# Performance work log

Measured on AMD Instinct MI355X. Metric: run time of the kernel, lower is better.

## Reference

```python
import jax, jax.numpy as jnp
import numpy as np

BATCH = 4096
VOCAB = 50257


def setup_inputs() -> dict:
    key = jax.random.key(0)
    k1, k2 = jax.random.split(key)
    pred = jax.random.normal(k1, (BATCH, VOCAB), dtype=jnp.float32)
    y = jax.random.randint(k2, (BATCH,), 0, VOCAB, dtype=jnp.int64)
    return {"pred": pred, "y": y}


def reference(pred, y):
    # Mean over batch of -log( exp(pred[i, y[i]]) / sum_j exp(pred[i, j]) )
    # == mean of -(log_softmax(pred)[i, y[i]]). Stable log-softmax is
    # mathematically identical to the original's unstabilized form.
    logp = jax.nn.log_softmax(pred, axis=-1)              # [B, V]
    picked = jnp.take_along_axis(logp, y[:, None], axis=-1)[:, 0]  # [B]
    return -jnp.mean(picked)
```

## Files before the change

### kernel.cpp

```cpp
#include <hip/hip_runtime.h>
#include <cstdint>

#define CE_BATCH 4096
#define CE_VOCAB 50257

__global__ __launch_bounds__(256, 4) void ce_kernel(const float* __restrict__ pred,
                                                    const int* __restrict__ y,
                                                    float* __restrict__ out) {
    const int b = blockIdx.x;
    const float* __restrict__ row = pred + (size_t)b * CE_VOCAB;
    const int tid = threadIdx.x;

    float m = -INFINITY;
    float s0 = 0.0f, s1 = 0.0f, s2 = 0.0f, s3 = 0.0f;
    float s4 = 0.0f, s5 = 0.0f, s6 = 0.0f, s7 = 0.0f;

    int lead = (int)(((16u - ((uintptr_t)row & 15u)) & 15u) >> 2);
    if (lead > CE_VOCAB) lead = CE_VOCAB;
    if (tid < lead) {
        m = row[tid];
        s0 = 1.0f;
    }

    const int nvec = (CE_VOCAB - lead) >> 2;
    const float4* __restrict__ vrow = (const float4*)(row + lead);

    int i = tid;
    for (; i + 7 * 256 < nvec; i += 8 * 256) {
        float4 v0 = vrow[i];
        float4 v1 = vrow[i + 1 * 256];
        float4 v2 = vrow[i + 2 * 256];
        float4 v3 = vrow[i + 3 * 256];
        float4 v4 = vrow[i + 4 * 256];
        float4 v5 = vrow[i + 5 * 256];
        float4 v6 = vrow[i + 6 * 256];
        float4 v7 = vrow[i + 7 * 256];

        float m0 = fmaxf(fmaxf(v0.x, v0.y), fmaxf(v0.z, v0.w));
        float m1 = fmaxf(fmaxf(v1.x, v1.y), fmaxf(v1.z, v1.w));
        float m2 = fmaxf(fmaxf(v2.x, v2.y), fmaxf(v2.z, v2.w));
        float m3 = fmaxf(fmaxf(v3.x, v3.y), fmaxf(v3.z, v3.w));
        float m4 = fmaxf(fmaxf(v4.x, v4.y), fmaxf(v4.z, v4.w));
        float m5 = fmaxf(fmaxf(v5.x, v5.y), fmaxf(v5.z, v5.w));
        float m6 = fmaxf(fmaxf(v6.x, v6.y), fmaxf(v6.z, v6.w));
        float m7 = fmaxf(fmaxf(v7.x, v7.y), fmaxf(v7.z, v7.w));
        float g = fmaxf(fmaxf(fmaxf(m0, m1), fmaxf(m2, m3)),
                        fmaxf(fmaxf(m4, m5), fmaxf(m6, m7)));

        if (g > m) {
            float r = __expf(m - g);
            s0 *= r; s1 *= r; s2 *= r; s3 *= r;
            s4 *= r; s5 *= r; s6 *= r; s7 *= r;
            m = g;
        }

        s0 += (__expf(v0.x - m) + __expf(v0.y - m)) + (__expf(v0.z - m) + __expf(v0.w - m));
        s1 += (__expf(v1.x - m) + __expf(v1.y - m)) + (__expf(v1.z - m) + __expf(v1.w - m));
        s2 += (__expf(v2.x - m) + __expf(v2.y - m)) + (__expf(v2.z - m) + __expf(v2.w - m));
        s3 += (__expf(v3.x - m) + __expf(v3.y - m)) + (__expf(v3.z - m) + __expf(v3.w - m));
        s4 += (__expf(v4.x - m) + __expf(v4.y - m)) + (__expf(v4.z - m) + __expf(v4.w - m));
        s5 += (__expf(v5.x - m) + __expf(v5.y - m)) + (__expf(v5.z - m) + __expf(v5.w - m));
        s6 += (__expf(v6.x - m) + __expf(v6.y - m)) + (__expf(v6.z - m) + __expf(v6.w - m));
        s7 += (__expf(v7.x - m) + __expf(v7.y - m)) + (__expf(v7.z - m) + __expf(v7.w - m));
    }

    for (; i < nvec; i += 256) {
        float4 v = vrow[i];
        float g = fmaxf(fmaxf(v.x, v.y), fmaxf(v.z, v.w));
        if (g > m) {
            float r = __expf(m - g);
            s0 *= r; s1 *= r; s2 *= r; s3 *= r;
            s4 *= r; s5 *= r; s6 *= r; s7 *= r;
            m = g;
        }
        s0 += (__expf(v.x - m) + __expf(v.y - m)) + (__expf(v.z - m) + __expf(v.w - m));
    }

    int t = lead + (nvec << 2) + tid;
    if (t < CE_VOCAB) {
        float x = row[t];
        if (x > m) {
            float r = __expf(m - x);
            s0 *= r; s1 *= r; s2 *= r; s3 *= r;
            s4 *= r; s5 *= r; s6 *= r; s7 *= r;
            m = x;
        }
        s0 += __expf(x - m);
    }

    float s = ((s0 + s1) + (s2 + s3)) + ((s4 + s5) + (s6 + s7));

    #pragma unroll
    for (int off = 1; off < 64; off <<= 1) {
        float om = __shfl_xor(m, off, 64);
        float os = __shfl_xor(s, off, 64);
        float nm = fmaxf(m, om);
        s = s * __expf(m - nm) + os * __expf(om - nm);
        m = nm;
    }

    __shared__ float sm[4];
    __shared__ float ss[4];
    const int wave = tid >> 6;
    if ((tid & 63) == 0) {
        sm[wave] = m;
        ss[wave] = s;
    }
    __syncthreads();

    if (tid == 0) {
        m = sm[0];
        s = ss[0];
        #pragma unroll
        for (int w = 1; w < 4; ++w) {
            float om = sm[w], os = ss[w];
            float nm = fmaxf(m, om);
            s = s * __expf(m - nm) + os * __expf(om - nm);
            m = nm;
        }
        float lse = m + __logf(s);
        float loss = lse - row[y[b]];
        atomicAdd(out, loss * (1.0f / CE_BATCH));
    }
}

extern "C" void kernel_launch(void* const* d_in, const int* in_sizes, int n_in,
                              void* d_out, int out_size, void* d_ws, size_t ws_size,
                              hipStream_t stream) {
    const float* pred = (const float*)d_in[0];
    const int* y = (const int*)d_in[1];
    float* out = (float*)d_out;

    hipMemsetAsync(out, 0, sizeof(float), stream);

    ce_kernel<<<CE_BATCH, 256, 0, stream>>>(pred, y, out);
}
```

Baseline: 1.018 ms.

## Give each wave a contiguous row chunk with nontemporal loads and higher occupancy

Each row is now split into four contiguous chunks, one per wave, and each wave streams its chunk with 64-lane strides instead of the block striding the whole row. Loads use nontemporal builtins, the unroll drops from 8 to 4 vectors, and launch bounds ask for 8 blocks per CU to cut register pressure and raise occupancy. The aim is better DRAM streaming and more waves in flight to hide latency. In exchange each thread has fewer loads in flight, and the per-wave access pattern changes.

```diff
diff --git a/kernel.cpp b/kernel.cpp
--- a/kernel.cpp
+++ b/kernel.cpp
@@ -4,16 +4,19 @@
 #define CE_BATCH 4096
 #define CE_VOCAB 50257
 
-__global__ __launch_bounds__(256, 4) void ce_kernel(const float* __restrict__ pred,
+typedef float f32x4 __attribute__((ext_vector_type(4)));
+
+__global__ __launch_bounds__(256, 8) void ce_kernel(const float* __restrict__ pred,
                                                     const int* __restrict__ y,
                                                     float* __restrict__ out) {
     const int b = blockIdx.x;
     const float* __restrict__ row = pred + (size_t)b * CE_VOCAB;
     const int tid = threadIdx.x;
+    const int wave = tid >> 6;
+    const int lane = tid & 63;
 
     float m = -INFINITY;
     float s0 = 0.0f, s1 = 0.0f, s2 = 0.0f, s3 = 0.0f;
-    float s4 = 0.0f, s5 = 0.0f, s6 = 0.0f, s7 = 0.0f;
 
     int lead = (int)(((16u - ((uintptr_t)row & 15u)) & 15u) >> 2);
     if (lead > CE_VOCAB) lead = CE_VOCAB;
@@ -23,34 +26,29 @@
     }
 
     const int nvec = (CE_VOCAB - lead) >> 2;
-    const float4* __restrict__ vrow = (const float4*)(row + lead);
+    const f32x4* __restrict__ vrow = (const f32x4*)(row + lead);
 
-    int i = tid;
-    for (; i + 7 * 256 < nvec; i += 8 * 256) {
-        float4 v0 = vrow[i];
-        float4 v1 = vrow[i + 1 * 256];
-        float4 v2 = vrow[i + 2 * 256];
-        float4 v3 = vrow[i + 3 * 256];
-        float4 v4 = vrow[i + 4 * 256];
-        float4 v5 = vrow[i + 5 * 256];
-        float4 v6 = vrow[i + 6 * 256];
-        float4 v7 = vrow[i + 7 * 256];
+    const int chunk = (nvec + 3) >> 2;
+    const int wbeg = wave * chunk;
+    const int wend0 = wbeg + chunk;
+    const int wend = wend0 < nvec ? wend0 : nvec;
+
+    int i = wbeg + lane;
+    for (; i + 3 * 64 < wend; i += 4 * 64) {
+        f32x4 v0 = __builtin_nontemporal_load(vrow + i);
+        f32x4 v1 = __builtin_nontemporal_load(vrow + i + 64);
+        f32x4 v2 = __builtin_nontemporal_load(vrow + i + 128);
+        f32x4 v3 = __builtin_nontemporal_load(vrow + i + 192);
 
         float m0 = fmaxf(fmaxf(v0.x, v0.y), fmaxf(v0.z, v0.w));
         float m1 = fmaxf(fmaxf(v1.x, v1.y), fmaxf(v1.z, v1.w));
         float m2 = fmaxf(fmaxf(v2.x, v2.y), fmaxf(v2.z, v2.w));
         float m3 = fmaxf(fmaxf(v3.x, v3.y), fmaxf(v3.z, v3.w));
-        float m4 = fmaxf(fmaxf(v4.x, v4.y), fmaxf(v4.z, v4.w));
-        float m5 = fmaxf(fmaxf(v5.x, v5.y), fmaxf(v5.z, v5.w));
-        float m6 = fmaxf(fmaxf(v6.x, v6.y), fmaxf(v6.z, v6.w));
-        float m7 = fmaxf(fmaxf(v7.x, v7.y), fmaxf(v7.z, v7.w));
-        float g = fmaxf(fmaxf(fmaxf(m0, m1), fmaxf(m2, m3)),
-                        fmaxf(fmaxf(m4, m5), fmaxf(m6, m7)));
+        float g = fmaxf(fmaxf(m0, m1), fmaxf(m2, m3));
 
         if (g > m) {
             float r = __expf(m - g);
             s0 *= r; s1 *= r; s2 *= r; s3 *= r;
-            s4 *= r; s5 *= r; s6 *= r; s7 *= r;
             m = g;
         }
 
@@ -58,19 +56,14 @@
         s1 += (__expf(v1.x - m) + __expf(v1.y - m)) + (__expf(v1.z - m) + __expf(v1.w - m));
         s2 += (__expf(v2.x - m) + __expf(v2.y - m)) + (__expf(v2.z - m) + __expf(v2.w - m));
         s3 += (__expf(v3.x - m) + __expf(v3.y - m)) + (__expf(v3.z - m) + __expf(v3.w - m));
-        s4 += (__expf(v4.x - m) + __expf(v4.y - m)) + (__expf(v4.z - m) + __expf(v4.w - m));
-        s5 += (__expf(v5.x - m) + __expf(v5.y - m)) + (__expf(v5.z - m) + __expf(v5.w - m));
-        s6 += (__expf(v6.x - m) + __expf(v6.y - m)) + (__expf(v6.z - m) + __expf(v6.w - m));
-        s7 += (__expf(v7.x - m) + __expf(v7.y - m)) + (__expf(v7.z - m) + __expf(v7.w - m));
     }
 
-    for (; i < nvec; i += 256) {
-        float4 v = vrow[i];
+    for (; i < wend; i += 64) {
+        f32x4 v = __builtin_nontemporal_load(vrow + i);
         float g = fmaxf(fmaxf(v.x, v.y), fmaxf(v.z, v.w));
         if (g > m) {
             float r = __expf(m - g);
             s0 *= r; s1 *= r; s2 *= r; s3 *= r;
-            s4 *= r; s5 *= r; s6 *= r; s7 *= r;
             m = g;
         }
         s0 += (__expf(v.x - m) + __expf(v.y - m)) + (__expf(v.z - m) + __expf(v.w - m));
@@ -82,13 +75,12 @@
         if (x > m) {
             float r = __expf(m - x);
             s0 *= r; s1 *= r; s2 *= r; s3 *= r;
-            s4 *= r; s5 *= r; s6 *= r; s7 *= r;
             m = x;
         }
         s0 += __expf(x - m);
     }
 
-    float s = ((s0 + s1) + (s2 + s3)) + ((s4 + s5) + (s6 + s7));
+    float s = (s0 + s1) + (s2 + s3);
 
     #pragma unroll
     for (int off = 1; off < 64; off <<= 1) {
@@ -101,7 +93,6 @@
 
     __shared__ float sm[4];
     __shared__ float ss[4];
-    const int wave = tid >> 6;
     if ((tid & 63) == 0) {
         sm[wave] = m;
         ss[wave] = s;
```

Result: faster. 994.4 us (-2.3%).
